# Kernel optimization log

Hardware: AMD Instinct MI355X
Metric: run time of the kernel (lower is better)

## Reference

```python
import jax, jax.numpy as jnp
import numpy as np

B, S = 32, 4096          # decode batch, kv cache length
HID, H = 5120, 16        # hidden size, local heads
DN, DR, DV = 128, 64, 128  # qk_nope, qk_rope, v head dims
QL, KL = 1536, 512       # q_lora_rank, kv_lora_rank
BASE = 10000.0
EPS = 1e-6
SCALE = (DN + DR) ** -0.5


def rmsnorm(x, w):
    return x * jax.lax.rsqrt(jnp.mean(x * x, axis=-1, keepdims=True) + EPS) * w


def rope_interleaved(x, pos):
    # non-neox (interleaved pairs) rope, per-row positions pos: [B]
    d = x.shape[-1]
    inv = 1.0 / (BASE ** (jnp.arange(0, d, 2, dtype=jnp.float32) / d))  # [d/2]
    fr = pos.astype(jnp.float32)[:, None] * inv                          # [B, d/2]
    cos, sin = jnp.cos(fr), jnp.sin(fr)
    x1, x2 = x[..., 0::2], x[..., 1::2]
    while cos.ndim < x1.ndim:  # broadcast over head dim if present
        cos, sin = cos[:, None], sin[:, None]
    o1 = x1 * cos - x2 * sin
    o2 = x2 * cos + x1 * sin
    return jnp.stack([o1, o2], axis=-1).reshape(x.shape)


def setup_inputs() -> dict:
    key = jax.random.key(0)
    ks = jax.random.split(key, 9)
    w = 0.02  # weight scale for sane activations
    return {
        "hidden_states": jax.random.normal(ks[0], (B, HID), jnp.float32),
        "positions": jax.random.randint(ks[1], (B,), 0, S, jnp.int32),
        "kv_cache_latent": jax.random.normal(ks[2], (B, S, KL), jnp.float32),
        "kv_cache_rope": jax.random.normal(ks[3], (B, S, DR), jnp.float32),
        "w_qkv_a": jax.random.normal(ks[4], (HID, QL + KL + DR), jnp.float32) * w,
        "q_a_norm_w": jnp.ones((QL,), jnp.float32),
        "w_q_b": jax.random.normal(ks[5], (QL, H * (DN + DR)), jnp.float32) * w,
        "kv_a_norm_w": jnp.ones((KL,), jnp.float32),
        "w_kc": jax.random.normal(ks[6], (H, DN, KL), jnp.float32) * w,
        "w_vc": jax.random.normal(ks[7], (H, KL, DV), jnp.float32) * w,
        "w_o": jax.random.normal(ks[8], (H * DV, HID), jnp.float32) * w,
    }


def reference(hidden_states, positions, kv_cache_latent, kv_cache_rope,
              w_qkv_a, q_a_norm_w, w_q_b, kv_a_norm_w, w_kc, w_vc, w_o):
    # fused qkv_a projection -> q_lora | kv latent | k_pe
    qkv = hidden_states @ w_qkv_a                       # [B, QL+KL+DR]
    q_a, latent, k_pe = jnp.split(qkv, [QL, QL + KL], axis=-1)

    # q path: rmsnorm -> q_b_proj -> per-head split nope/pe
    q = (rmsnorm(q_a, q_a_norm_w) @ w_q_b).reshape(B, H, DN + DR)
    q_nope, q_pe = q[..., :DN], q[..., DN:]
    q_pe = rope_interleaved(q_pe, positions)            # [B, H, DR]

    # kv latent path: rmsnorm latent, rope k_pe, write current token into cache
    latent_n = rmsnorm(latent, kv_a_norm_w)             # [B, KL]
    k_pe = rope_interleaved(k_pe, positions)            # [B, DR]
    cache_l = kv_cache_latent.at[:, -1, :].set(latent_n)  # [B, S, KL]
    cache_r = kv_cache_rope.at[:, -1, :].set(k_pe)        # [B, S, DR]

    # weight absorption: q_nope absorbed through w_kc into latent space
    q_abs = jnp.einsum("bhd,hdc->bhc", q_nope, w_kc)    # [B, H, KL]

    # MQA attention over latent KV (1 kv head shared by all q heads)
    scores = (jnp.einsum("bhc,bsc->bhs", q_abs, cache_l)
              + jnp.einsum("bhr,bsr->bhs", q_pe, cache_r)) * SCALE
    attn = jax.nn.softmax(scores, axis=-1)              # [B, H, S]
    ctx = jnp.einsum("bhs,bsc->bhc", attn, cache_l)     # [B, H, KL]

    # un-absorb values through w_vc, then output projection
    out = jnp.einsum("bhc,hcv->bhv", ctx, w_vc).reshape(B, H * DV)
    return out @ w_o                                    # [B, HID]
```

## Files before the change

kernel.cpp:

```cpp
#include <hip/hip_runtime.h>
#include <hip/hip_bf16.h>
#include <stdint.h>

#define B_   32
#define S_   4096
#define HID_ 5120
#define H_   16
#define DN_  128
#define DR_  64
#define DV_  128
#define QL_  1536
#define KL_  512
#define KC_  576
#define NQKV_ 2112
#define NQB_  3072
#define EPS_ 1e-6f
#define SCALE_ 0.07216878364870323f

typedef __attribute__((ext_vector_type(4))) float f32x4;
typedef __attribute__((ext_vector_type(8))) short s16x8;
typedef __attribute__((ext_vector_type(2))) unsigned int u32x2;
typedef __attribute__((ext_vector_type(4))) unsigned int u32x4;

__device__ __forceinline__ unsigned short bf(float f) {
  union { __hip_bfloat16 h; unsigned short u; } v;
  v.h = __float2bfloat16(f);
  return v.u;
}
__device__ __forceinline__ unsigned int bf2(float x, float y) {
  union { __hip_bfloat162 h; unsigned int u; } v;
  v.h = __float22bfloat162_rn(float2{x, y});
  return v.u;
}
__device__ __forceinline__ s16x8 pack8(const float* w) {
  union { u32x4 q; s16x8 s; } v;
  v.q = (u32x4){bf2(w[0], w[1]), bf2(w[2], w[3]), bf2(w[4], w[5]), bf2(w[6], w[7])};
  return v.s;
}

__device__ __forceinline__ u32x2 ds_tr16(unsigned addr) {
  u32x2 d;
  asm volatile("ds_read_b64_tr_b16 %0, %1" : "=v"(d) : "v"(addr));
  return d;
}

template<int K, int TK, int N>
__global__ __launch_bounds__(256) void gemm_bf(const unsigned short* __restrict__ Abf,
                                               const float* __restrict__ W,
                                               float* __restrict__ P) {
  int t = threadIdx.x, wave = t >> 6, lane = t & 63;
  int quad = lane >> 4, lo = lane & 15;
  int n0 = blockIdx.x * 64 + wave * 16;
  int k0 = blockIdx.y * TK;
  f32x4 acc0 = {0.f, 0.f, 0.f, 0.f}, acc1 = {0.f, 0.f, 0.f, 0.f};
  const float* wp = W + (size_t)(k0 + quad * 8) * N + n0 + lo;
  const unsigned short* a0p = Abf + (size_t)lo * K + k0 + quad * 8;
  const unsigned short* a1p = Abf + (size_t)(16 + lo) * K + k0 + quad * 8;
#pragma unroll 2
  for (int kk = 0; kk < TK / 32; ++kk) {
    s16x8 a0 = *(const s16x8*)(a0p + kk * 32);
    s16x8 a1 = *(const s16x8*)(a1p + kk * 32);
    float wv[8];
#pragma unroll
    for (int j = 0; j < 8; ++j) wv[j] = wp[((size_t)kk * 32 + j) * N];
    s16x8 bfv = pack8(wv);
    acc0 = __builtin_amdgcn_mfma_f32_16x16x32_bf16(a0, bfv, acc0, 0, 0, 0);
    acc1 = __builtin_amdgcn_mfma_f32_16x16x32_bf16(a1, bfv, acc1, 0, 0, 0);
  }
  float* p = P + ((size_t)blockIdx.y * B_) * N + n0 + lo;
#pragma unroll
  for (int reg = 0; reg < 4; ++reg) {
    p[(size_t)(quad * 4 + reg) * N]      = acc0[reg];
    p[(size_t)(16 + quad * 4 + reg) * N] = acc1[reg];
  }
}

template<int K, int TK, int N>
__global__ __launch_bounds__(256) void gemm_f32a(const float* __restrict__ A,
                                                 const float* __restrict__ W,
                                                 float* __restrict__ P) {
  int t = threadIdx.x, wave = t >> 6, lane = t & 63;
  int quad = lane >> 4, lo = lane & 15;
  int n0 = blockIdx.x * 64 + wave * 16;
  int k0 = blockIdx.y * TK;
  f32x4 acc0 = {0.f, 0.f, 0.f, 0.f}, acc1 = {0.f, 0.f, 0.f, 0.f};
  const float* wp = W + (size_t)(k0 + quad * 8) * N + n0 + lo;
  const float* a0p = A + (size_t)lo * K + k0 + quad * 8;
  const float* a1p = A + (size_t)(16 + lo) * K + k0 + quad * 8;
#pragma unroll 2
  for (int kk = 0; kk < TK / 32; ++kk) {
    f32x4 x0 = *(const f32x4*)(a0p + kk * 32);
    f32x4 x1 = *(const f32x4*)(a0p + kk * 32 + 4);
    f32x4 y0 = *(const f32x4*)(a1p + kk * 32);
    f32x4 y1 = *(const f32x4*)(a1p + kk * 32 + 4);
    float a0f[8], a1f[8];
#pragma unroll
    for (int j = 0; j < 4; ++j) {
      a0f[j] = x0[j]; a0f[4 + j] = x1[j];
      a1f[j] = y0[j]; a1f[4 + j] = y1[j];
    }
    s16x8 a0 = pack8(a0f);
    s16x8 a1 = pack8(a1f);
    float wv[8];
#pragma unroll
    for (int j = 0; j < 8; ++j) wv[j] = wp[((size_t)kk * 32 + j) * N];
    s16x8 bfv = pack8(wv);
    acc0 = __builtin_amdgcn_mfma_f32_16x16x32_bf16(a0, bfv, acc0, 0, 0, 0);
    acc1 = __builtin_amdgcn_mfma_f32_16x16x32_bf16(a1, bfv, acc1, 0, 0, 0);
  }
  float* p = P + ((size_t)blockIdx.y * B_) * N + n0 + lo;
#pragma unroll
  for (int reg = 0; reg < 4; ++reg) {
    p[(size_t)(quad * 4 + reg) * N]      = acc0[reg];
    p[(size_t)(16 + quad * 4 + reg) * N] = acc1[reg];
  }
}

#define NSL1 32
#define NSL2 24
#define NSL3 16

__global__ __launch_bounds__(256) void k2a(const float* __restrict__ P1, const float* __restrict__ qw,
                    const float* __restrict__ kvw, const int* __restrict__ pos,
                    unsigned short* __restrict__ qn_bf, float* __restrict__ latent_n,
                    float* __restrict__ kpe_rot, float* __restrict__ cs_buf) {
  int b = blockIdx.y, t = threadIdx.x;
  __shared__ float row[QL_];
  __shared__ float red[256];
  if (blockIdx.x == 0) {
    float sq = 0.f;
    for (int n = t; n < QL_; n += 256) {
      float s = 0.f;
#pragma unroll
      for (int ks = 0; ks < NSL1; ++ks) s += P1[((size_t)ks * B_ + b) * NQKV_ + n];
      row[n] = s; sq += s * s;
    }
    red[t] = sq;
    __syncthreads();
    for (int off = 128; off > 0; off >>= 1) {
      if (t < off) red[t] += red[t + off];
      __syncthreads();
    }
    float rq = 1.0f / sqrtf(red[0] / QL_ + EPS_);
    for (int n = t; n < QL_; n += 256) qn_bf[(size_t)b * QL_ + n] = bf(row[n] * rq * qw[n]);
  } else {
    float sl = 0.f;
    for (int n = t; n < KL_ + DR_; n += 256) {
      float s = 0.f;
#pragma unroll
      for (int ks = 0; ks < NSL1; ++ks) s += P1[((size_t)ks * B_ + b) * NQKV_ + QL_ + n];
      row[n] = s;
      if (n < KL_) sl += s * s;
    }
    red[t] = sl;
    __syncthreads();
    for (int off = 128; off > 0; off >>= 1) {
      if (t < off) red[t] += red[t + off];
      __syncthreads();
    }
    float rl = 1.0f / sqrtf(red[0] / KL_ + EPS_);
    for (int n = t; n < KL_; n += 256) latent_n[(size_t)b * KL_ + n] = row[n] * rl * kvw[n];
    if (t < 32) {
      double inv = exp(-((double)t / 32.0) * log(10000.0));
      float fr = (float)pos[b] * (float)inv;
      float c = (float)cos((double)fr), s = (float)sin((double)fr);
      cs_buf[(b * 32 + t) * 2] = c; cs_buf[(b * 32 + t) * 2 + 1] = s;
      float x1 = row[KL_ + 2 * t], x2 = row[KL_ + 2 * t + 1];
      kpe_rot[b * DR_ + 2 * t]     = x1 * c - x2 * s;
      kpe_rot[b * DR_ + 2 * t + 1] = x2 * c + x1 * s;
    }
  }
}

__global__ __launch_bounds__(256) void k2c(const float* __restrict__ P2,
                                           const float* __restrict__ w_kc,
                                           const float* __restrict__ cs_buf,
                                           unsigned short* __restrict__ q_cat) {
  int b = blockIdx.y, t = threadIdx.x, wave = t >> 6, lane = t & 63;
  int hl = blockIdx.x * 2;
  __shared__ float qh[2][192];
  for (int j = t; j < 384; j += 256) {
    int hh = j / 192, jj = j - hh * 192;
    float s = 0.f;
    int col = (hl + hh) * 192 + jj;
#pragma unroll
    for (int ks = 0; ks < NSL2; ++ks) s += P2[((size_t)ks * B_ + b) * NQB_ + col];
    qh[hh][jj] = s;
  }
  __syncthreads();
  if (t < 64) {
    int hh = t >> 5, ll = t & 31;
    float c = cs_buf[(b * 32 + ll) * 2], s = cs_buf[(b * 32 + ll) * 2 + 1];
    float x1 = qh[hh][DN_ + 2 * ll], x2 = qh[hh][DN_ + 2 * ll + 1];
    qh[hh][DN_ + 2 * ll]     = x1 * c - x2 * s;
    qh[hh][DN_ + 2 * ll + 1] = x2 * c + x1 * s;
  }
  __syncthreads();
  int hh = wave >> 1, half = wave & 1;
  int h = hl + hh;
  float acc[4] = {0.f, 0.f, 0.f, 0.f};
  const float* wk = w_kc + (size_t)h * DN_ * KL_ + half * 256;
#pragma unroll 2
  for (int d = 0; d < DN_; ++d) {
    float qd = qh[hh][d];
#pragma unroll
    for (int i = 0; i < 4; ++i)
      acc[i] = fmaf(qd, wk[(size_t)d * KL_ + lane + 64 * i], acc[i]);
  }
  unsigned short* qc = q_cat + ((size_t)b * H_ + h) * KC_;
#pragma unroll
  for (int i = 0; i < 4; ++i) qc[half * 256 + lane + 64 * i] = bf(acc[i] * SCALE_);
  if (half == 0) qc[KL_ + lane] = bf(qh[hh][DN_ + lane] * SCALE_);
}

#define CHUNK_ 256
#define TR_ 32
#define NTL_ 8
#define NSUB_ 36

__global__ __launch_bounds__(256, 2) void attn(
    const float* __restrict__ cache_l, const float* __restrict__ cache_r,
    const float* __restrict__ latent_n, const float* __restrict__ kpe_rot,
    const unsigned short* __restrict__ q_cat,
    float* __restrict__ ws_acc, float* __restrict__ ws_ml) {
  int chunk = blockIdx.x, b = blockIdx.y;
  int t = threadIdx.x, wave = t >> 6, lane = t & 63;
  int quad = lane >> 4, lo = lane & 15;

  __shared__ __attribute__((aligned(16))) unsigned short Lt[8 * NSUB_ * 64];
  __shared__ __attribute__((aligned(16))) unsigned short pb[4][H_ * TR_];

  s16x8 af[18];
  const unsigned short* qc = q_cat + ((size_t)b * H_ + lo) * KC_;
#pragma unroll
  for (int ks = 0; ks < 18; ++ks) af[ks] = *(const s16x8*)(qc + ks * 32 + quad * 8);

  f32x4 accc[NTL_];
#pragma unroll
  for (int i = 0; i < NTL_; ++i) accc[i] = (f32x4){0.f, 0.f, 0.f, 0.f};
  float m_run[4], l_run[4];
#pragma unroll
  for (int r = 0; r < 4; ++r) { m_run[r] = -3.0e38f; l_run[r] = 0.f; }

  int r8 = t >> 3, u = t & 7;

  u32x2 o[18];
  auto load_tile = [&](int tile) {
    int s = chunk * CHUNK_ + tile * TR_ + r8;
    const float* rl = cache_l + ((size_t)b * S_ + s) * KL_;
    const float* rr = cache_r + ((size_t)b * S_ + s) * DR_;
    if (s == S_ - 1) { rl = latent_n + (size_t)b * KL_; rr = kpe_rot + (size_t)b * DR_; }
#pragma unroll
    for (int j = 0; j < 18; ++j) {
      int c = u * 4 + j * 32;
      float4 v = *(const float4*)((j < 16) ? (rl + c) : (rr + (c - 512)));
      o[j][0] = bf2(v.x, v.y); o[j][1] = bf2(v.z, v.w);
    }
  };
  load_tile(0);

  unsigned ltb = (unsigned)(size_t)(&Lt[0]);

#pragma unroll 1
  for (int tile = 0; tile < NTL_; ++tile) {
    __syncthreads();
#pragma unroll
    for (int j = 0; j < 18; ++j) {
      int c = u * 4 + j * 32;
      int e = ((r8 >> 2) * NSUB_ + (c >> 4)) * 64 + (r8 & 3) * 16 + (c & 15);
      *(u32x2*)(&Lt[e]) = o[j];
    }
    if (tile + 1 < NTL_) load_tile(tile + 1);
    __syncthreads();

    f32x4 sc0 = {0.f, 0.f, 0.f, 0.f}, sc1 = {0.f, 0.f, 0.f, 0.f};
#pragma unroll
    for (int ks = 0; ks < 18; ++ks) {
      int e0 = ((lo >> 2) * NSUB_ + 2 * ks + (quad >> 1)) * 64 + (lo & 3) * 16 + 8 * (quad & 1);
      s16x8 b0 = *(const s16x8*)(&Lt[e0]);
      s16x8 b1 = *(const s16x8*)(&Lt[e0 + 4 * NSUB_ * 64]);
      sc0 = __builtin_amdgcn_mfma_f32_16x16x32_bf16(af[ks], b0, sc0, 0, 0, 0);
      sc1 = __builtin_amdgcn_mfma_f32_16x16x32_bf16(af[ks], b1, sc1, 0, 0, 0);
    }

#pragma unroll
    for (int reg = 0; reg < 4; ++reg) {
      float s0 = sc0[reg], s1 = sc1[reg];
      float mt = fmaxf(s0, s1);
#pragma unroll
      for (int m = 1; m < 16; m <<= 1) mt = fmaxf(mt, __shfl_xor(mt, m, 64));
      float mn = fmaxf(m_run[reg], mt);
      float alpha = __expf(m_run[reg] - mn);
      m_run[reg] = mn;
      float p0 = __expf(s0 - mn), p1 = __expf(s1 - mn);
      float lt = p0 + p1;
#pragma unroll
      for (int m = 1; m < 16; m <<= 1) lt += __shfl_xor(lt, m, 64);
      l_run[reg] = l_run[reg] * alpha + lt;
#pragma unroll
      for (int i = 0; i < NTL_; ++i) accc[i][reg] *= alpha;
      int h = quad * 4 + reg;
      pb[wave][h * TR_ + lo]      = bf(p0);
      pb[wave][h * TR_ + 16 + lo] = bf(p1);
    }
    s16x8 ap = *(const s16x8*)(&pb[wave][lo * TR_ + quad * 8]);

    u32x2 r0[NTL_], r1[NTL_];
#pragma unroll
    for (int nt = 0; nt < NTL_; ++nt) {
      unsigned base = ltb + (unsigned)((((quad * 2) * NSUB_ + wave * 8 + nt) * 64) * 2 + lo * 8);
      r0[nt] = ds_tr16(base);
      r1[nt] = ds_tr16(base + NSUB_ * 128);
    }
    asm volatile("s_waitcnt lgkmcnt(0)" ::: "memory");
    __builtin_amdgcn_sched_barrier(0);
#pragma unroll
    for (int nt = 0; nt < NTL_; ++nt) {
      union { u32x2 d[2]; s16x8 s; } bb;
      bb.d[0] = r0[nt]; bb.d[1] = r1[nt];
      accc[nt] = __builtin_amdgcn_mfma_f32_16x16x32_bf16(ap, bb.s, accc[nt], 0, 0, 0);
    }
  }

  float* accp = ws_acc + (((size_t)b * 16 + chunk) * H_) * KL_;
#pragma unroll
  for (int nt = 0; nt < NTL_; ++nt) {
    int c = wave * 128 + nt * 16 + lo;
#pragma unroll
    for (int reg = 0; reg < 4; ++reg)
      accp[(size_t)(quad * 4 + reg) * KL_ + c] = accc[nt][reg];
  }
  if (wave == 0 && lo == 0) {
#pragma unroll
    for (int reg = 0; reg < 4; ++reg) {
      int h = quad * 4 + reg;
      ws_ml[(((size_t)b * 16 + chunk) * H_ + h) * 2 + 0] = m_run[reg];
      ws_ml[(((size_t)b * 16 + chunk) * H_ + h) * 2 + 1] = l_run[reg];
    }
  }
}

__global__ __launch_bounds__(256) void combine(const float* __restrict__ ws_acc,
                        const float* __restrict__ ws_ml,
                        const float* __restrict__ w_vc, unsigned short* __restrict__ o_v) {
  int h = blockIdx.x, b = blockIdx.y, t = threadIdx.x;
  __shared__ float sm[16], sl[16];
  __shared__ float ctx[KL_];
  __shared__ float ps[256];
  if (t < 16) {
    sm[t] = ws_ml[(((size_t)b * 16 + t) * H_ + h) * 2];
    sl[t] = ws_ml[(((size_t)b * 16 + t) * H_ + h) * 2 + 1];
  }
  __syncthreads();
  float M = -3e38f;
#pragma unroll
  for (int i = 0; i < 16; ++i) M = fmaxf(M, sm[i]);
  float wkk[16]; float Lsum = 0.f;
#pragma unroll
  for (int i = 0; i < 16; ++i) { wkk[i] = __expf(sm[i] - M); Lsum += wkk[i] * sl[i]; }
  float invL = 1.0f / Lsum;
  for (int c = t; c < KL_; c += 256) {
    float s = 0.f;
#pragma unroll
    for (int i = 0; i < 16; ++i)
      s += wkk[i] * ws_acc[(((size_t)b * 16 + i) * H_ + h) * KL_ + c];
    ctx[c] = s * invL;
  }
  __syncthreads();
  int vv = t & 127, half = t >> 7;
  const float* wv = w_vc + (size_t)h * KL_ * DV_;
  float s0 = 0.f, s1 = 0.f;
#pragma unroll 4
  for (int k = half * 256; k < half * 256 + 256; k += 2) {
    s0 = fmaf(ctx[k],     wv[(size_t)k * DV_ + vv],       s0);
    s1 = fmaf(ctx[k + 1], wv[(size_t)(k + 1) * DV_ + vv], s1);
  }
  ps[t] = s0 + s1;
  __syncthreads();
  if (t < 128) o_v[(size_t)b * (H_ * DV_) + h * DV_ + t] = bf(ps[t] + ps[t + 128]);
}

__global__ __launch_bounds__(256) void reduce_out(const float* __restrict__ P, float* __restrict__ out) {
  int i = blockIdx.x * 256 + threadIdx.x;
  const f32x4* P4 = (const f32x4*)P;
  f32x4 s = P4[i];
#pragma unroll
  for (int ks = 1; ks < NSL3; ++ks) s += P4[(size_t)ks * 40960 + i];
  ((f32x4*)out)[i] = s;
}

extern "C" void kernel_launch(void* const* d_in, const int* in_sizes, int n_in,
                              void* d_out, int out_size, void* d_ws, size_t ws_size,
                              hipStream_t stream) {
  const float* hs    = (const float*)d_in[0];
  const int*   pos   = (const int*)d_in[1];
  const float* cl    = (const float*)d_in[2];
  const float* cr    = (const float*)d_in[3];
  const float* w_qkv = (const float*)d_in[4];
  const float* qnw   = (const float*)d_in[5];
  const float* w_qb  = (const float*)d_in[6];
  const float* kvnw  = (const float*)d_in[7];
  const float* w_kc  = (const float*)d_in[8];
  const float* w_vc  = (const float*)d_in[9];
  const float* w_o   = (const float*)d_in[10];
  float* out = (float*)d_out;

  char* ws = (char*)d_ws;
  float* ws_acc = (float*)(ws);
  float* P1     = (float*)(ws + 16777216);
  float* P2     = (float*)(ws + 25427968);
  float* P5     = (float*)(ws + 34865152);
  unsigned short* qn_bf = (unsigned short*)(ws + 45350912);
  float* latent_n = (float*)(ws + 45449216);
  float* kpe_rot  = (float*)(ws + 45514752);
  float* cs_buf   = (float*)(ws + 45522944);
  unsigned short* q_cat = (unsigned short*)(ws + 45531136);
  float* ws_ml    = (float*)(ws + 46120960);
  unsigned short* o_v_bf = (unsigned short*)(ws + 46186496);

  gemm_f32a<HID_, 160, NQKV_><<<dim3(33, 32), 256, 0, stream>>>(hs, w_qkv, P1);
  k2a<<<dim3(2, 32), 256, 0, stream>>>(P1, qnw, kvnw, pos, qn_bf, latent_n, kpe_rot, cs_buf);
  gemm_bf<QL_, 64, NQB_><<<dim3(48, 24), 256, 0, stream>>>(qn_bf, w_qb, P2);
  k2c<<<dim3(8, 32), 256, 0, stream>>>(P2, w_kc, cs_buf, q_cat);
  attn<<<dim3(16, 32), 256, 0, stream>>>(cl, cr, latent_n, kpe_rot, q_cat, ws_acc, ws_ml);
  combine<<<dim3(16, 32), 256, 0, stream>>>(ws_acc, ws_ml, w_vc, o_v_bf);
  gemm_bf<H_ * DV_, 128, HID_><<<dim3(80, 16), 256, 0, stream>>>(o_v_bf, w_o, P5);
  reduce_out<<<160, 256, 0, stream>>>(P5, out);
}
```

Measured before the change: 551.8 us.

## Stage weight tiles through LDS with async global-to-LDS double buffering

The two GEMM kernels now preload all activation fragments into registers and stream the fp32 weight tile through shared memory. Each step issues direct global-to-LDS 16-byte loads into a double buffer, then reads it back per wave. The old per-lane strided scalar weight reads become coalesced row loads, and the next tile's fetch can overlap the current MFMA. In exchange it adds a block barrier every k-step, more registers for the unrolled A fragments, and relies on the async LDS loads completing before the barrier without explicit vmcnt waits.

```diff
diff --git a/kernel.cpp b/kernel.cpp
--- a/kernel.cpp
+++ b/kernel.cpp
@@ -44,30 +44,58 @@
   return d;
 }
 
+__device__ __forceinline__ void gload_lds16(const float* g, float* l) {
+  __builtin_amdgcn_global_load_lds((const void __attribute__((address_space(1)))*)g,
+                                   (void __attribute__((address_space(3)))*)l, 16, 0, 0);
+}
+
 template<int K, int TK, int N>
 __global__ __launch_bounds__(256) void gemm_bf(const unsigned short* __restrict__ Abf,
                                                const float* __restrict__ W,
                                                float* __restrict__ P) {
+  constexpr int NI = TK / 32;
+  __shared__ __attribute__((aligned(16))) float Wt[2][2048];
   int t = threadIdx.x, wave = t >> 6, lane = t & 63;
   int quad = lane >> 4, lo = lane & 15;
-  int n0 = blockIdx.x * 64 + wave * 16;
+  int nb = blockIdx.x * 64;
   int k0 = blockIdx.y * TK;
-  f32x4 acc0 = {0.f, 0.f, 0.f, 0.f}, acc1 = {0.f, 0.f, 0.f, 0.f};
-  const float* wp = W + (size_t)(k0 + quad * 8) * N + n0 + lo;
+
+  s16x8 a0[NI], a1[NI];
   const unsigned short* a0p = Abf + (size_t)lo * K + k0 + quad * 8;
   const unsigned short* a1p = Abf + (size_t)(16 + lo) * K + k0 + quad * 8;
-#pragma unroll 2
-  for (int kk = 0; kk < TK / 32; ++kk) {
-    s16x8 a0 = *(const s16x8*)(a0p + kk * 32);
-    s16x8 a1 = *(const s16x8*)(a1p + kk * 32);
+#pragma unroll
+  for (int kk = 0; kk < NI; ++kk) {
+    a0[kk] = *(const s16x8*)(a0p + kk * 32);
+    a1[kk] = *(const s16x8*)(a1p + kk * 32);
+  }
+
+  auto stage = [&](int buf, int kk) {
+    int g0 = k0 + kk * 32;
+#pragma unroll
+    for (int i = 0; i < 2; ++i) {
+      const float* gp = W + (size_t)(g0 + i * 16 + wave * 4 + (lane >> 4)) * N
+                          + nb + (lane & 15) * 4;
+      gload_lds16(gp, &Wt[buf][i * 1024 + wave * 256]);
+    }
+  };
+
+  stage(0, 0);
+  __syncthreads();
+
+  f32x4 acc0 = {0.f, 0.f, 0.f, 0.f}, acc1 = {0.f, 0.f, 0.f, 0.f};
+#pragma unroll
+  for (int kk = 0; kk < NI; ++kk) {
+    if (kk + 1 < NI) stage((kk + 1) & 1, kk + 1);
+    const float* wrow = &Wt[kk & 1][wave * 16 + lo];
     float wv[8];
 #pragma unroll
-    for (int j = 0; j < 8; ++j) wv[j] = wp[((size_t)kk * 32 + j) * N];
+    for (int j = 0; j < 8; ++j) wv[j] = wrow[(quad * 8 + j) * 64];
     s16x8 bfv = pack8(wv);
-    acc0 = __builtin_amdgcn_mfma_f32_16x16x32_bf16(a0, bfv, acc0, 0, 0, 0);
-    acc1 = __builtin_amdgcn_mfma_f32_16x16x32_bf16(a1, bfv, acc1, 0, 0, 0);
-  }
-  float* p = P + ((size_t)blockIdx.y * B_) * N + n0 + lo;
+    acc0 = __builtin_amdgcn_mfma_f32_16x16x32_bf16(a0[kk], bfv, acc0, 0, 0, 0);
+    acc1 = __builtin_amdgcn_mfma_f32_16x16x32_bf16(a1[kk], bfv, acc1, 0, 0, 0);
+    __syncthreads();
+  }
+  float* p = P + ((size_t)blockIdx.y * B_) * N + nb + wave * 16 + lo;
 #pragma unroll
   for (int reg = 0; reg < 4; ++reg) {
     p[(size_t)(quad * 4 + reg) * N]      = acc0[reg];
@@ -79,16 +107,18 @@
 __global__ __launch_bounds__(256) void gemm_f32a(const float* __restrict__ A,
                                                  const float* __restrict__ W,
                                                  float* __restrict__ P) {
+  constexpr int NI = TK / 32;
+  __shared__ __attribute__((aligned(16))) float Wt[2][2048];
   int t = threadIdx.x, wave = t >> 6, lane = t & 63;
   int quad = lane >> 4, lo = lane & 15;
-  int n0 = blockIdx.x * 64 + wave * 16;
+  int nb = blockIdx.x * 64;
   int k0 = blockIdx.y * TK;
-  f32x4 acc0 = {0.f, 0.f, 0.f, 0.f}, acc1 = {0.f, 0.f, 0.f, 0.f};
-  const float* wp = W + (size_t)(k0 + quad * 8) * N + n0 + lo;
+
+  s16x8 a0[NI], a1[NI];
   const float* a0p = A + (size_t)lo * K + k0 + quad * 8;
   const float* a1p = A + (size_t)(16 + lo) * K + k0 + quad * 8;
-#pragma unroll 2
-  for (int kk = 0; kk < TK / 32; ++kk) {
+#pragma unroll
+  for (int kk = 0; kk < NI; ++kk) {
     f32x4 x0 = *(const f32x4*)(a0p + kk * 32);
     f32x4 x1 = *(const f32x4*)(a0p + kk * 32 + 4);
     f32x4 y0 = *(const f32x4*)(a1p + kk * 32);
@@ -99,16 +129,37 @@
       a0f[j] = x0[j]; a0f[4 + j] = x1[j];
       a1f[j] = y0[j]; a1f[4 + j] = y1[j];
     }
-    s16x8 a0 = pack8(a0f);
-    s16x8 a1 = pack8(a1f);
+    a0[kk] = pack8(a0f);
+    a1[kk] = pack8(a1f);
+  }
+
+  auto stage = [&](int buf, int kk) {
+    int g0 = k0 + kk * 32;
+#pragma unroll
+    for (int i = 0; i < 2; ++i) {
+      const float* gp = W + (size_t)(g0 + i * 16 + wave * 4 + (lane >> 4)) * N
+                          + nb + (lane & 15) * 4;
+      gload_lds16(gp, &Wt[buf][i * 1024 + wave * 256]);
+    }
+  };
+
+  stage(0, 0);
+  __syncthreads();
+
+  f32x4 acc0 = {0.f, 0.f, 0.f, 0.f}, acc1 = {0.f, 0.f, 0.f, 0.f};
+#pragma unroll
+  for (int kk = 0; kk < NI; ++kk) {
+    if (kk + 1 < NI) stage((kk + 1) & 1, kk + 1);
+    const float* wrow = &Wt[kk & 1][wave * 16 + lo];
     float wv[8];
 #pragma unroll
-    for (int j = 0; j < 8; ++j) wv[j] = wp[((size_t)kk * 32 + j) * N];
+    for (int j = 0; j < 8; ++j) wv[j] = wrow[(quad * 8 + j) * 64];
     s16x8 bfv = pack8(wv);
-    acc0 = __builtin_amdgcn_mfma_f32_16x16x32_bf16(a0, bfv, acc0, 0, 0, 0);
-    acc1 = __builtin_amdgcn_mfma_f32_16x16x32_bf16(a1, bfv, acc1, 0, 0, 0);
-  }
-  float* p = P + ((size_t)blockIdx.y * B_) * N + n0 + lo;
+    acc0 = __builtin_amdgcn_mfma_f32_16x16x32_bf16(a0[kk], bfv, acc0, 0, 0, 0);
+    acc1 = __builtin_amdgcn_mfma_f32_16x16x32_bf16(a1[kk], bfv, acc1, 0, 0, 0);
+    __syncthreads();
+  }
+  float* p = P + ((size_t)blockIdx.y * B_) * N + nb + wave * 16 + lo;
 #pragma unroll
   for (int reg = 0; reg < 4; ++reg) {
     p[(size_t)(quad * 4 + reg) * N]      = acc0[reg];
```

New measurement: 551.5 us. About the same (-0.1%).
